# Optimization experiments

Measured on AMD Instinct MI355X. Metric: run time of the kernel, lower is better.

Reference implementation:

```python
import jax, jax.numpy as jnp
import numpy as np

N = 50000
E = 800000
D = 128
BOND = 64


def setup_inputs() -> dict:
    key = jax.random.key(0)
    ks = jax.random.split(key, 8)
    h = jax.random.normal(ks[0], (N, D), dtype=jnp.float32)
    edge_index = jax.random.randint(ks[1], (2, E), 0, N, dtype=jnp.int64)
    bond_emb = jax.random.normal(ks[2], (E, BOND), dtype=jnp.float32)
    # node_update: Linear(2D+64 -> D), ReLU, Linear(D -> D)
    lim1 = 1.0 / np.sqrt(2 * D + BOND)
    W1 = jax.random.uniform(ks[3], (2 * D + BOND, D), minval=-lim1, maxval=lim1, dtype=jnp.float32)
    b1 = jnp.zeros((D,), dtype=jnp.float32)
    lim2 = 1.0 / np.sqrt(D)
    W2 = jax.random.uniform(ks[4], (D, D), minval=-lim2, maxval=lim2, dtype=jnp.float32)
    b2 = jnp.zeros((D,), dtype=jnp.float32)
    # bond_attention: Linear(64 -> 1)
    lim3 = 1.0 / np.sqrt(BOND)
    Wa = jax.random.uniform(ks[5], (BOND, 1), minval=-lim3, maxval=lim3, dtype=jnp.float32)
    ba = jnp.zeros((1,), dtype=jnp.float32)
    return {"h": h, "edge_index": edge_index, "bond_emb": bond_emb,
            "W1": W1, "b1": b1, "W2": W2, "b2": b2, "Wa": Wa, "ba": ba}


def reference(h, edge_index, bond_emb, W1, b1, W2, b2, Wa, ba):
    row, col = edge_index[0], edge_index[1]
    # sigmoid gate per edge: [E, 1]
    bond_weights = jax.nn.sigmoid(bond_emb @ Wa + ba)
    # gather + concat: [E, 2D + 64]
    messages = jnp.concatenate([h[row], h[col], bond_emb], axis=-1)
    # MLP: Linear -> ReLU -> Linear, then gate
    messages = jax.nn.relu(messages @ W1 + b1) @ W2 + b2
    messages = messages * bond_weights
    # scatter-add into destination nodes (index_add_ on row)
    h_new = jax.ops.segment_sum(messages, row, num_segments=h.shape[0])
    return h + h_new
```

## Files before the change

### kernel.cpp

```cpp
#include <hip/hip_runtime.h>
#include <math.h>

#define NN 50000
#define NE 800000
#define NB1 196
#define NTILES 25000
#define TT 7
#define EDGE_BLOCKS 512
#define LDSF 64

typedef __attribute__((ext_vector_type(8))) short short8;
typedef __attribute__((ext_vector_type(4))) float f32x4;

__device__ __forceinline__ unsigned short f2bf(float f) {
    __bf16 b = (__bf16)f;
    return __builtin_bit_cast(unsigned short, b);
}

__device__ __forceinline__ short8 pack8(float4 a, float4 b) {
    short8 s;
    s[0] = (short)f2bf(a.x); s[1] = (short)f2bf(a.y);
    s[2] = (short)f2bf(a.z); s[3] = (short)f2bf(a.w);
    s[4] = (short)f2bf(b.x); s[5] = (short)f2bf(b.y);
    s[6] = (short)f2bf(b.z); s[7] = (short)f2bf(b.w);
    return s;
}

__device__ __forceinline__ int clampi(int v, int hi) {
    return v < 0 ? 0 : (v > hi ? hi : v);
}

__device__ __forceinline__ bool sniff_i64(const int* ei) {
    return ((ei[1] | ei[3] | ei[5] | ei[7] | ei[9] | ei[11] | ei[13] | ei[15]) == 0);
}

__global__ void pack_weights_kernel(const float* __restrict__ W1, const float* __restrict__ W2,
                                    unsigned short* __restrict__ w1p, unsigned short* __restrict__ w2n) {
    int idx = blockIdx.x * 256 + threadIdx.x;
    if (idx < 320 * 128) {
        int e = idx & 7, lane = (idx >> 3) & 63, f = idx >> 9;
        int tm = f & 7, ks = f >> 3;
        int k = ks * 32 + 8 * (lane >> 4) + e;
        int n = tm * 16 + (lane & 15);
        w1p[idx] = f2bf(W1[k * 128 + n]);
    }
    if (idx < 128 * 128) {
        int e = idx & 7, lane = (idx >> 3) & 63, f = idx >> 9;
        int tn = f & 7, ks = f >> 3;
        int k = ks * 32 + 8 * (lane >> 4) + e;
        int n = tn * 16 + (lane & 15);
        w2n[idx] = f2bf(W2[k * 128 + n]);
    }
}

__global__ void pack_w1_kernel(const float* __restrict__ W1, unsigned short* __restrict__ outp) {
    int idx = blockIdx.x * 256 + threadIdx.x;
    if (idx >= 320 * 128) return;
    int e = idx & 7, lane = (idx >> 3) & 63, f = idx >> 9;
    int tm = f & 7, ks = f >> 3;
    int k = ks * 32 + 8 * (lane >> 4) + e;
    int n = tm * 16 + (lane & 15);
    outp[idx] = f2bf(W1[k * 128 + n]);
}

__global__ void pack_w2_kernel(const float* __restrict__ W2, unsigned short* __restrict__ outp) {
    int idx = blockIdx.x * 256 + threadIdx.x;
    if (idx >= 128 * 128) return;
    int e = idx & 7, lane = (idx >> 3) & 63, f = idx >> 9;
    int tn = f & 7, ks2 = f >> 3;
    int k = (2 * ks2 + (e >> 2)) * 16 + 4 * (lane >> 4) + (e & 3);
    int n = tn * 16 + (lane & 15);
    outp[idx] = f2bf(W2[k * 128 + n]);
}

__global__ void prep_kernel(const float4* __restrict__ h, ushort4* __restrict__ hbf,
                            float4* __restrict__ s, float* __restrict__ G,
                            int* __restrict__ cnt) {
    int i = blockIdx.x * 256 + threadIdx.x;
    int stride = gridDim.x * 256;
    for (int j = i; j < NN * 32; j += stride) {
        float4 f = h[j];
        ushort4 u;
        u.x = f2bf(f.x); u.y = f2bf(f.y); u.z = f2bf(f.z); u.w = f2bf(f.w);
        hbf[j] = u;
        s[j] = (float4){0.f, 0.f, 0.f, 0.f};
    }
    for (int j = i; j < NN; j += stride) { G[j] = 0.f; cnt[j] = 0; }
}

__global__ void copy_h_kernel(const float4* __restrict__ h, float4* __restrict__ outp) {
    int i = blockIdx.x * 256 + threadIdx.x;
    int stride = gridDim.x * 256;
    for (; i < NN * 32; i += stride) outp[i] = h[i];
}

__global__ void hist_kernel(const int* __restrict__ ei, int* __restrict__ cnt) {
    const bool i64 = sniff_i64(ei);
    const long long* ei64 = (const long long*)ei;
    for (int e = blockIdx.x * 256 + threadIdx.x; e < NE; e += gridDim.x * 256) {
        int r = i64 ? (int)ei64[e] : ei[e];
        r = clampi(r, NN - 1);
        atomicAdd(&cnt[r], 1);
    }
}

__global__ void scan1_kernel(const int* __restrict__ cnt, int* __restrict__ scanned,
                             int* __restrict__ bsum) {
    __shared__ int sm[256];
    int b = blockIdx.x, t = threadIdx.x, i = b * 256 + t;
    int c = (i < NN) ? cnt[i] : 0;
    sm[t] = c; __syncthreads();
#pragma unroll
    for (int d = 1; d < 256; d <<= 1) {
        int x = (t >= d) ? sm[t - d] : 0;
        __syncthreads();
        sm[t] += x;
        __syncthreads();
    }
    if (i < NN) scanned[i] = sm[t] - c;
    if (t == 255) bsum[b] = sm[255];
}

__global__ void scan2_kernel(const int* __restrict__ bsum, int* __restrict__ boff) {
    __shared__ int sm[256];
    int t = threadIdx.x;
    int c = (t < NB1) ? bsum[t] : 0;
    sm[t] = c; __syncthreads();
#pragma unroll
    for (int d = 1; d < 256; d <<= 1) {
        int x = (t >= d) ? sm[t - d] : 0;
        __syncthreads();
        sm[t] += x;
        __syncthreads();
    }
    if (t < NB1) boff[t] = sm[t] - c;
}

__global__ void scan3_kernel(const int* __restrict__ scanned, const int* __restrict__ boff,
                             int* __restrict__ cur) {
    int b = blockIdx.x, t = threadIdx.x, i = b * 256 + t;
    if (i < NN) cur[i] = scanned[i] + boff[b];
}

__global__ void scatter_kernel(const int* __restrict__ ei, int* __restrict__ cur,
                               int4* __restrict__ recs) {
    const bool i64 = sniff_i64(ei);
    const long long* ei64 = (const long long*)ei;
    for (int e = blockIdx.x * 256 + threadIdx.x; e < NE; e += gridDim.x * 256) {
        int r, c;
        if (i64) { r = (int)ei64[e]; c = (int)ei64[NE + e]; }
        else     { r = ei[e];        c = ei[NE + e]; }
        r = clampi(r, NN - 1);
        c = clampi(c, NN - 1);
        int pos = atomicAdd(&cur[r], 1);
        pos = clampi(pos, NE - 1);
        recs[pos] = make_int4(r, c, e, 0);
    }
}

__global__ __launch_bounds__(512) void edge_kernel_sorted(
    const unsigned short* __restrict__ hbf, const int4* __restrict__ recs,
    const float* __restrict__ bond, const float* __restrict__ b1v,
    const float* __restrict__ Wa, const float* __restrict__ bav,
    const short8* __restrict__ w1p, float* __restrict__ s, float* __restrict__ G)
{
    __shared__ short8 ldsW1[LDSF * 64];
    const int tid = threadIdx.x;
    for (int i = tid; i < LDSF * 64; i += 512) ldsW1[i] = w1p[i];
    __syncthreads();

    const int lane = tid & 63;
    const int g = lane >> 4;
    const int m = lane & 15;
    const float baS = bav[0];

    int bid = blockIdx.x;
    bid = (bid & 7) * (EDGE_BLOCKS / 8) + (bid >> 3);
    const int gw = bid * 8 + (tid >> 6);
    const int t0 = gw * TT;
    int myT = NTILES - t0;
    if (myT > 0) {
        if (myT > TT) myT = TT;
        const long wbase = (long)t0 * 32;
        const int qst = 8 * myT;
        const long colBase = wbase + (long)(m >> 2) * qst + (m & 3);

        int cn = -1;
        float cg = 0.f;
        float cv[8];
#pragma unroll
        for (int tm = 0; tm < 8; ++tm) cv[tm] = 0.f;

        for (int t = 0; t < myT; ++t) {
            int rA[2], cA[2], eO[2];
#pragma unroll
            for (int nt = 0; nt < 2; ++nt) {
                int4 rec = recs[colBase + t * 8 + nt * 4];
                rA[nt] = clampi(rec.x, NN - 1);
                cA[nt] = clampi(rec.y, NN - 1);
                eO[nt] = clampi(rec.z, NE - 1);
            }

            f32x4 acc1[8][2];
#pragma unroll
            for (int tm = 0; tm < 8; ++tm)
#pragma unroll
                for (int nt = 0; nt < 2; ++nt)
                    acc1[tm][nt] = (f32x4){0.f, 0.f, 0.f, 0.f};
            float gp[2] = {0.f, 0.f};

#pragma unroll
            for (int ks = 0; ks < 10; ++ks) {
                short8 bf[2];
#pragma unroll
                for (int nt = 0; nt < 2; ++nt) {
                    if (ks < 8) {
                        int node = (ks < 4) ? rA[nt] : cA[nt];
                        const unsigned short* p = hbf + (long)node * 128 + (ks & 3) * 32 + 8 * g;
                        bf[nt] = *(const short8*)p;
                    } else {
                        const float* p = bond + (long)eO[nt] * 64 + (ks - 8) * 32 + 8 * g;
                        float4 f0 = *(const float4*)(p);
                        float4 f1 = *(const float4*)(p + 4);
                        bf[nt] = pack8(f0, f1);
                        const float* wap = Wa + (ks - 8) * 32 + 8 * g;
                        float4 w0 = *(const float4*)(wap);
                        float4 w1q = *(const float4*)(wap + 4);
                        gp[nt] += f0.x * w0.x + f0.y * w0.y + f0.z * w0.z + f0.w * w0.w
                                + f1.x * w1q.x + f1.y * w1q.y + f1.z * w1q.z + f1.w * w1q.w;
                    }
                }
#pragma unroll
                for (int tm = 0; tm < 8; ++tm) {
                    const int f = ks * 8 + tm;
                    short8 wfrag = (f < LDSF) ? ldsW1[f * 64 + lane] : w1p[f * 64 + lane];
                    acc1[tm][0] = __builtin_amdgcn_mfma_f32_16x16x32_bf16(bf[0], wfrag, acc1[tm][0], 0, 0, 0);
                    acc1[tm][1] = __builtin_amdgcn_mfma_f32_16x16x32_bf16(bf[1], wfrag, acc1[tm][1], 0, 0, 0);
                }
            }

            float gate[2];
#pragma unroll
            for (int nt = 0; nt < 2; ++nt) {
                float ssum = gp[nt];
                ssum += __shfl_xor(ssum, 16);
                ssum += __shfl_xor(ssum, 32);
                gate[nt] = 1.f / (1.f + expf(-(ssum + baS)));
            }

#pragma unroll
            for (int nt = 0; nt < 2; ++nt) {
#pragma unroll
                for (int r = 0; r < 4; ++r) {
                    int nd = __shfl(rA[nt], 4 * g + r);
                    float gr = __shfl(gate[nt], 4 * g + r);
                    if (nd == cn) {
#pragma unroll
                        for (int tm = 0; tm < 8; ++tm)
                            cv[tm] += fmaxf(acc1[tm][nt][r] + b1v[tm * 16 + m], 0.f) * gr;
                        cg += gr;
                    } else {
                        if (cn >= 0) {
#pragma unroll
                            for (int tm = 0; tm < 8; ++tm)
                                atomicAdd(s + (long)cn * 128 + tm * 16 + m, cv[tm]);
                            if (m == 0) atomicAdd(G + cn, cg);
                        }
                        cn = nd;
#pragma unroll
                        for (int tm = 0; tm < 8; ++tm)
                            cv[tm] = fmaxf(acc1[tm][nt][r] + b1v[tm * 16 + m], 0.f) * gr;
                        cg = gr;
                    }
                }
            }
        }

        if (cn >= 0) {
#pragma unroll
            for (int tm = 0; tm < 8; ++tm)
                atomicAdd(s + (long)cn * 128 + tm * 16 + m, cv[tm]);
            if (m == 0) atomicAdd(G + cn, cg);
        }
    }
}

__global__ __launch_bounds__(256) void final_mfma_kernel(
    const float* __restrict__ h, const float* __restrict__ G,
    const float* __restrict__ b2v, const short8* __restrict__ w2n,
    float* __restrict__ sout)
{
    const int tid = threadIdx.x;
    const int lane = tid & 63;
    const int g = lane >> 4;
    const int m = lane & 15;
    const int wtile = blockIdx.x * 4 + (tid >> 6);
    if (wtile >= NN / 16) return;
    const int n0 = wtile * 16;

    f32x4 acc[8];
#pragma unroll
    for (int tn = 0; tn < 8; ++tn) {
#pragma unroll
        for (int r = 0; r < 4; ++r) {
            int n = n0 + 4 * g + r;
            int d = tn * 16 + m;
            acc[tn][r] = h[(long)n * 128 + d] + G[n] * b2v[d];
        }
    }

#pragma unroll
    for (int ks = 0; ks < 4; ++ks) {
        const float* sp = sout + (long)(n0 + m) * 128 + ks * 32 + 8 * g;
        float4 f0 = *(const float4*)(sp);
        float4 f1 = *(const float4*)(sp + 4);
        short8 a = pack8(f0, f1);
#pragma unroll
        for (int tn = 0; tn < 8; ++tn)
            acc[tn] = __builtin_amdgcn_mfma_f32_16x16x32_bf16(a, w2n[(ks * 8 + tn) * 64 + lane], acc[tn], 0, 0, 0);
    }

#pragma unroll
    for (int tn = 0; tn < 8; ++tn)
#pragma unroll
        for (int r = 0; r < 4; ++r)
            sout[(long)(n0 + 4 * g + r) * 128 + tn * 16 + m] = acc[tn][r];
}

__global__ __launch_bounds__(512) void edge_kernel_unsorted(
    const float* __restrict__ h, const int* __restrict__ ei,
    const float* __restrict__ bond, const float* __restrict__ b1v,
    const float* __restrict__ b2v, const float* __restrict__ Wa,
    const float* __restrict__ bav, const short8* __restrict__ w1p,
    const short8* __restrict__ w2p, float* __restrict__ outp)
{
    __shared__ short8 ldsW1[5120];
    const int tid = threadIdx.x;
#pragma unroll
    for (int i = 0; i < 10; ++i) ldsW1[tid + i * 512] = w1p[tid + i * 512];
    __syncthreads();

    const int lane = tid & 63;
    const int g = lane >> 4;
    const int m = lane & 15;
    const float baS = bav[0];
    const long long* ei64 = (const long long*)ei;
    const bool i64 = sniff_i64(ei);

    const int gw = blockIdx.x * 8 + (tid >> 6);
    const int nw = gridDim.x * 8;
    for (int tile = gw; tile < NE / 32; tile += nw) {
        const int eb = tile * 32;
        int eIdx[2], rA[2], cA[2];
#pragma unroll
        for (int nt = 0; nt < 2; ++nt) {
            eIdx[nt] = eb + nt * 16 + m;
            if (i64) { rA[nt] = (int)ei64[eIdx[nt]]; cA[nt] = (int)ei64[NE + eIdx[nt]]; }
            else     { rA[nt] = ei[eIdx[nt]];        cA[nt] = ei[NE + eIdx[nt]]; }
            rA[nt] = clampi(rA[nt], NN - 1);
            cA[nt] = clampi(cA[nt], NN - 1);
        }
        f32x4 acc1[8][2];
#pragma unroll
        for (int tm = 0; tm < 8; ++tm)
#pragma unroll
            for (int nt = 0; nt < 2; ++nt) acc1[tm][nt] = (f32x4){0.f,0.f,0.f,0.f};
        float gp[2] = {0.f, 0.f};
#pragma unroll
        for (int ks = 0; ks < 10; ++ks) {
            short8 bf[2];
#pragma unroll
            for (int nt = 0; nt < 2; ++nt) {
                const float* p;
                if (ks < 4)      p = h + (long)rA[nt] * 128 + ks * 32;
                else if (ks < 8) p = h + (long)cA[nt] * 128 + (ks - 4) * 32;
                else             p = bond + (long)eIdx[nt] * 64 + (ks - 8) * 32;
                float4 f0 = *(const float4*)(p + 8 * g);
                float4 f1 = *(const float4*)(p + 8 * g + 4);
                bf[nt] = pack8(f0, f1);
                if (ks >= 8) {
                    const float* wap = Wa + (ks - 8) * 32 + 8 * g;
                    float4 w0 = *(const float4*)(wap);
                    float4 w1q = *(const float4*)(wap + 4);
                    gp[nt] += f0.x * w0.x + f0.y * w0.y + f0.z * w0.z + f0.w * w0.w
                            + f1.x * w1q.x + f1.y * w1q.y + f1.z * w1q.z + f1.w * w1q.w;
                }
            }
#pragma unroll
            for (int tm = 0; tm < 8; ++tm) {
                short8 a = ldsW1[(ks * 8 + tm) * 64 + lane];
                acc1[tm][0] = __builtin_amdgcn_mfma_f32_16x16x32_bf16(a, bf[0], acc1[tm][0], 0, 0, 0);
                acc1[tm][1] = __builtin_amdgcn_mfma_f32_16x16x32_bf16(a, bf[1], acc1[tm][1], 0, 0, 0);
            }
        }
        float gate[2];
#pragma unroll
        for (int nt = 0; nt < 2; ++nt) {
            float ssum = gp[nt];
            ssum += __shfl_xor(ssum, 16);
            ssum += __shfl_xor(ssum, 32);
            gate[nt] = 1.f / (1.f + expf(-(ssum + baS)));
        }
        short8 pf[4][2];
#pragma unroll
        for (int ks2 = 0; ks2 < 4; ++ks2) {
            float4 c0 = *(const float4*)(b1v + (2 * ks2) * 16 + 4 * g);
            float4 c1 = *(const float4*)(b1v + (2 * ks2 + 1) * 16 + 4 * g);
#pragma unroll
            for (int nt = 0; nt < 2; ++nt) {
                float4 lo, hi;
                lo.x = fmaxf(acc1[2*ks2][nt][0] + c0.x, 0.f);
                lo.y = fmaxf(acc1[2*ks2][nt][1] + c0.y, 0.f);
                lo.z = fmaxf(acc1[2*ks2][nt][2] + c0.z, 0.f);
                lo.w = fmaxf(acc1[2*ks2][nt][3] + c0.w, 0.f);
                hi.x = fmaxf(acc1[2*ks2+1][nt][0] + c1.x, 0.f);
                hi.y = fmaxf(acc1[2*ks2+1][nt][1] + c1.y, 0.f);
                hi.z = fmaxf(acc1[2*ks2+1][nt][2] + c1.z, 0.f);
                hi.w = fmaxf(acc1[2*ks2+1][nt][3] + c1.w, 0.f);
                pf[ks2][nt] = pack8(lo, hi);
            }
        }
        f32x4 acc2[8][2];
#pragma unroll
        for (int tn = 0; tn < 8; ++tn)
#pragma unroll
            for (int nt = 0; nt < 2; ++nt) acc2[tn][nt] = (f32x4){0.f,0.f,0.f,0.f};
#pragma unroll
        for (int ks2 = 0; ks2 < 4; ++ks2) {
#pragma unroll
            for (int tn = 0; tn < 8; ++tn) {
                short8 ww = w2p[(ks2 * 8 + tn) * 64 + lane];
                acc2[tn][0] = __builtin_amdgcn_mfma_f32_16x16x32_bf16(pf[ks2][0], ww, acc2[tn][0], 0, 0, 0);
                acc2[tn][1] = __builtin_amdgcn_mfma_f32_16x16x32_bf16(pf[ks2][1], ww, acc2[tn][1], 0, 0, 0);
            }
        }
#pragma unroll
        for (int nt = 0; nt < 2; ++nt) {
            int nodeR[4]; float gt[4];
#pragma unroll
            for (int r = 0; r < 4; ++r) {
                nodeR[r] = __shfl(rA[nt], 4 * g + r);
                gt[r] = __shfl(gate[nt], 4 * g + r);
            }
#pragma unroll
            for (int tn = 0; tn < 8; ++tn) {
                float c2 = b2v[tn * 16 + m];
#pragma unroll
                for (int r = 0; r < 4; ++r) {
                    float vv = (acc2[tn][nt][r] + c2) * gt[r];
                    atomicAdd(outp + (long)nodeR[r] * 128 + tn * 16 + m, vv);
                }
            }
        }
    }
}

extern "C" void kernel_launch(void* const* d_in, const int* in_sizes, int n_in,
                              void* d_out, int out_size, void* d_ws, size_t ws_size,
                              hipStream_t stream) {
    const float* h    = (const float*)d_in[0];
    const int*   ei   = (const int*)d_in[1];
    const float* bond = (const float*)d_in[2];
    const float* W1   = (const float*)d_in[3];
    const float* b1   = (const float*)d_in[4];
    const float* W2   = (const float*)d_in[5];
    const float* b2   = (const float*)d_in[6];
    const float* Wa   = (const float*)d_in[7];
    const float* ba   = (const float*)d_in[8];
    float* outp = (float*)d_out;

    char* ws = (char*)d_ws;
    const size_t o_w1  = 0;
    const size_t o_w2  = 81920;
    const size_t o_hbf = 114688;
    const size_t o_cnt = 12914688;
    const size_t o_scn = 13114688;
    const size_t o_bs  = 13314688;
    const size_t o_bo  = 13315712;
    const size_t o_cur = 13316736;
    const size_t o_rec = 13516736;
    const size_t need  = 26316736;

    unsigned short* w1p = (unsigned short*)(ws + o_w1);
    unsigned short* w2p = (unsigned short*)(ws + o_w2);

    if (ws_size >= need) {
        unsigned short* hbf = (unsigned short*)(ws + o_hbf);
        int* cnt = (int*)(ws + o_cnt);
        int* scn = (int*)(ws + o_scn);
        int* bs  = (int*)(ws + o_bs);
        int* bo  = (int*)(ws + o_bo);
        int* cur = (int*)(ws + o_cur);
        int4* recs = (int4*)(ws + o_rec);
        float* G = (float*)(ws + o_scn);

        hipLaunchKernelGGL(pack_weights_kernel, dim3(160), dim3(256), 0, stream, W1, W2, w1p, w2p);
        hipLaunchKernelGGL(prep_kernel, dim3(2048), dim3(256), 0, stream,
                           (const float4*)h, (ushort4*)hbf, (float4*)outp, G, cnt);
        hipLaunchKernelGGL(hist_kernel, dim3(1024), dim3(256), 0, stream, ei, cnt);
        hipLaunchKernelGGL(scan1_kernel, dim3(NB1), dim3(256), 0, stream, cnt, scn, bs);
        hipLaunchKernelGGL(scan2_kernel, dim3(1), dim3(256), 0, stream, bs, bo);
        hipLaunchKernelGGL(scan3_kernel, dim3(NB1), dim3(256), 0, stream, scn, bo, cur);
        hipLaunchKernelGGL(scatter_kernel, dim3(1024), dim3(256), 0, stream, ei, cur, recs);
        hipLaunchKernelGGL(edge_kernel_sorted, dim3(EDGE_BLOCKS), dim3(512), 0, stream,
                           hbf, recs, bond, b1, Wa, ba,
                           (const short8*)w1p, outp, G);
        hipLaunchKernelGGL(final_mfma_kernel, dim3((NN / 16 + 3) / 4), dim3(256), 0, stream,
                           h, G, b2, (const short8*)w2p, outp);
    } else {
        hipLaunchKernelGGL(pack_w1_kernel, dim3(160), dim3(256), 0, stream, W1, w1p);
        hipLaunchKernelGGL(pack_w2_kernel, dim3(64), dim3(256), 0, stream, W2, w2p);
        hipLaunchKernelGGL(copy_h_kernel, dim3(1600), dim3(256), 0, stream,
                           (const float4*)h, (float4*)outp);
        hipLaunchKernelGGL(edge_kernel_unsorted, dim3(512), dim3(512), 0, stream,
                           h, ei, bond, b1, b2, Wa, ba,
                           (const short8*)w1p, (const short8*)w2p, outp);
    }
}
```

Before: 248.8 us.

## Software-pipeline edge record and node-feature gathers across tile iterations

Prefetches the next tile's edge records and gathered bf16 node rows (row and col features) into registers while the current tile's MFMA chain and scatter epilogue run. Bond-embedding loads and gate dot products are hoisted ahead of the MFMA loop. The aim is to hide gather latency in the edge kernel. In exchange, register pressure rises (two sets of 16 short8 fragments plus accumulators), which may lower occupancy or cause spills.

New measurement: 277.9 us. +11.7%, slower.

```diff
diff --git a/kernel.cpp b/kernel.cpp
--- a/kernel.cpp
+++ b/kernel.cpp
@@ -191,15 +191,29 @@
 #pragma unroll
         for (int tm = 0; tm < 8; ++tm) cv[tm] = 0.f;
 
+        int rA[2], cA[2], eO[2];
+        short8 hb[2][8];
+#pragma unroll
+        for (int nt = 0; nt < 2; ++nt) {
+            int4 rc = recs[colBase + nt * 4];
+            rA[nt] = clampi(rc.x, NN - 1);
+            cA[nt] = clampi(rc.y, NN - 1);
+            eO[nt] = clampi(rc.z, NE - 1);
+        }
+#pragma unroll
+        for (int nt = 0; nt < 2; ++nt)
+#pragma unroll
+            for (int ks = 0; ks < 8; ++ks) {
+                int node = (ks < 4) ? rA[nt] : cA[nt];
+                hb[nt][ks] = *(const short8*)(hbf + (long)node * 128 + (ks & 3) * 32 + 8 * g);
+            }
+
         for (int t = 0; t < myT; ++t) {
-            int rA[2], cA[2], eO[2];
-#pragma unroll
-            for (int nt = 0; nt < 2; ++nt) {
-                int4 rec = recs[colBase + t * 8 + nt * 4];
-                rA[nt] = clampi(rec.x, NN - 1);
-                cA[nt] = clampi(rec.y, NN - 1);
-                eO[nt] = clampi(rec.z, NE - 1);
-            }
+            const int t1 = (t + 1 < myT) ? t + 1 : t;
+            int4 recN[2];
+#pragma unroll
+            for (int nt = 0; nt < 2; ++nt)
+                recN[nt] = recs[colBase + t1 * 8 + nt * 4];
 
             f32x4 acc1[8][2];
 #pragma unroll
@@ -207,37 +221,55 @@
 #pragma unroll
                 for (int nt = 0; nt < 2; ++nt)
                     acc1[tm][nt] = (f32x4){0.f, 0.f, 0.f, 0.f};
+
+            short8 bfb[2][2];
             float gp[2] = {0.f, 0.f};
+#pragma unroll
+            for (int nt = 0; nt < 2; ++nt)
+#pragma unroll
+                for (int kb = 0; kb < 2; ++kb) {
+                    const float* p = bond + (long)eO[nt] * 64 + kb * 32 + 8 * g;
+                    float4 f0 = *(const float4*)(p);
+                    float4 f1 = *(const float4*)(p + 4);
+                    bfb[nt][kb] = pack8(f0, f1);
+                    const float* wap = Wa + kb * 32 + 8 * g;
+                    float4 w0 = *(const float4*)(wap);
+                    float4 w1q = *(const float4*)(wap + 4);
+                    gp[nt] += f0.x * w0.x + f0.y * w0.y + f0.z * w0.z + f0.w * w0.w
+                            + f1.x * w1q.x + f1.y * w1q.y + f1.z * w1q.z + f1.w * w1q.w;
+                }
 
 #pragma unroll
             for (int ks = 0; ks < 10; ++ks) {
-                short8 bf[2];
-#pragma unroll
-                for (int nt = 0; nt < 2; ++nt) {
-                    if (ks < 8) {
-                        int node = (ks < 4) ? rA[nt] : cA[nt];
-                        const unsigned short* p = hbf + (long)node * 128 + (ks & 3) * 32 + 8 * g;
-                        bf[nt] = *(const short8*)p;
-                    } else {
-                        const float* p = bond + (long)eO[nt] * 64 + (ks - 8) * 32 + 8 * g;
-                        float4 f0 = *(const float4*)(p);
-                        float4 f1 = *(const float4*)(p + 4);
-                        bf[nt] = pack8(f0, f1);
-                        const float* wap = Wa + (ks - 8) * 32 + 8 * g;
-                        float4 w0 = *(const float4*)(wap);
-                        float4 w1q = *(const float4*)(wap + 4);
-                        gp[nt] += f0.x * w0.x + f0.y * w0.y + f0.z * w0.z + f0.w * w0.w
-                                + f1.x * w1q.x + f1.y * w1q.y + f1.z * w1q.z + f1.w * w1q.w;
-                    }
-                }
 #pragma unroll
                 for (int tm = 0; tm < 8; ++tm) {
                     const int f = ks * 8 + tm;
                     short8 wfrag = (f < LDSF) ? ldsW1[f * 64 + lane] : w1p[f * 64 + lane];
-                    acc1[tm][0] = __builtin_amdgcn_mfma_f32_16x16x32_bf16(bf[0], wfrag, acc1[tm][0], 0, 0, 0);
-                    acc1[tm][1] = __builtin_amdgcn_mfma_f32_16x16x32_bf16(bf[1], wfrag, acc1[tm][1], 0, 0, 0);
+                    if (ks < 8) {
+                        acc1[tm][0] = __builtin_amdgcn_mfma_f32_16x16x32_bf16(hb[0][ks], wfrag, acc1[tm][0], 0, 0, 0);
+                        acc1[tm][1] = __builtin_amdgcn_mfma_f32_16x16x32_bf16(hb[1][ks], wfrag, acc1[tm][1], 0, 0, 0);
+                    } else {
+                        acc1[tm][0] = __builtin_amdgcn_mfma_f32_16x16x32_bf16(bfb[0][ks - 8], wfrag, acc1[tm][0], 0, 0, 0);
+                        acc1[tm][1] = __builtin_amdgcn_mfma_f32_16x16x32_bf16(bfb[1][ks - 8], wfrag, acc1[tm][1], 0, 0, 0);
+                    }
                 }
             }
+
+            int rAN[2], cAN[2], eON[2];
+#pragma unroll
+            for (int nt = 0; nt < 2; ++nt) {
+                rAN[nt] = clampi(recN[nt].x, NN - 1);
+                cAN[nt] = clampi(recN[nt].y, NN - 1);
+                eON[nt] = clampi(recN[nt].z, NE - 1);
+            }
+            short8 hbN[2][8];
+#pragma unroll
+            for (int nt = 0; nt < 2; ++nt)
+#pragma unroll
+                for (int ks = 0; ks < 8; ++ks) {
+                    int node = (ks < 4) ? rAN[nt] : cAN[nt];
+                    hbN[nt][ks] = *(const short8*)(hbf + (long)node * 128 + (ks & 3) * 32 + 8 * g);
+                }
 
             float gate[2];
 #pragma unroll
@@ -273,6 +305,13 @@
                         cg = gr;
                     }
                 }
+            }
+
+#pragma unroll
+            for (int nt = 0; nt < 2; ++nt) {
+                rA[nt] = rAN[nt]; cA[nt] = cAN[nt]; eO[nt] = eON[nt];
+#pragma unroll
+                for (int ks = 0; ks < 8; ++ks) hb[nt][ks] = hbN[nt][ks];
             }
         }
 
```
